# Optimization experiments

Hardware: AMD Instinct MI355X
Metric: run time of the kernel (lower is better)

The kernel has to match this reference:

```python
import jax, jax.numpy as jnp
import numpy as np

N = 100000
E = 640000
ND = 128   # node_dim
ED = 128   # edge_dim
HD = 256   # hidden_dim
EPS = 1e-5


def _mlp_ln(x, W1, b1, W2, b2, W3, b3, g, beta):
    h = jax.nn.relu(x @ W1 + b1)
    h = jax.nn.relu(h @ W2 + b2)
    o = h @ W3 + b3
    mu = jnp.mean(o, axis=-1, keepdims=True)
    var = jnp.mean(jnp.square(o - mu), axis=-1, keepdims=True)
    return (o - mu) * jax.lax.rsqrt(var + EPS) * g + beta


def setup_inputs() -> dict:
    key = jax.random.key(0)
    ks = jax.random.split(key, 20)
    s = 0.02
    inp = {
        "node_emb": jax.random.normal(ks[0], (N, ND), jnp.float32),
        "edge_emb": jax.random.normal(ks[1], (E, ED), jnp.float32),
        "src": jax.random.randint(ks[2], (E,), 0, N),
        "dst": jax.random.randint(ks[3], (E,), 0, N),
        "num_nodes": N,
        # edge MLP: in = 2*ND + ED
        "eW1": jax.random.normal(ks[4], (2 * ND + ED, HD), jnp.float32) * s,
        "eb1": jnp.zeros((HD,), jnp.float32),
        "eW2": jax.random.normal(ks[5], (HD, HD), jnp.float32) * s,
        "eb2": jnp.zeros((HD,), jnp.float32),
        "eW3": jax.random.normal(ks[6], (HD, ED), jnp.float32) * s,
        "eb3": jnp.zeros((ED,), jnp.float32),
        "eg": jnp.ones((ED,), jnp.float32),
        "ebeta": jnp.zeros((ED,), jnp.float32),
        # node MLP: in = ND + ED
        "nW1": jax.random.normal(ks[7], (ND + ED, HD), jnp.float32) * s,
        "nb1": jnp.zeros((HD,), jnp.float32),
        "nW2": jax.random.normal(ks[8], (HD, HD), jnp.float32) * s,
        "nb2": jnp.zeros((HD,), jnp.float32),
        "nW3": jax.random.normal(ks[9], (HD, ND), jnp.float32) * s,
        "nb3": jnp.zeros((ND,), jnp.float32),
        "ng": jnp.ones((ND,), jnp.float32),
        "nbeta": jnp.zeros((ND,), jnp.float32),
    }
    return inp


def reference(node_emb, edge_emb, src, dst, num_nodes,
              eW1, eb1, eW2, eb2, eW3, eb3, eg, ebeta,
              nW1, nb1, nW2, nb2, nW3, nb3, ng, nbeta):
    # Edge update: e' = MLP(concat(h_i, h_j, e)) + e
    edge_input = jnp.concatenate([node_emb[src], node_emb[dst], edge_emb], axis=-1)
    edge_emb_new = _mlp_ln(edge_input, eW1, eb1, eW2, eb2, eW3, eb3, eg, ebeta) + edge_emb
    # Mean aggregation over incoming edges per dst node
    agg = jax.ops.segment_sum(edge_emb_new, dst, num_segments=num_nodes)
    count = jax.ops.segment_sum(jnp.ones((dst.shape[0], 1), node_emb.dtype), dst, num_segments=num_nodes)
    agg = agg / jnp.maximum(count, 1.0)
    # Node update: h' = MLP(concat(h, agg)) + h
    node_input = jnp.concatenate([node_emb, agg], axis=-1)
    node_emb_new = _mlp_ln(node_input, nW1, nb1, nW2, nb2, nW3, nb3, ng, nbeta) + node_emb
    return (node_emb_new, edge_emb_new)
```

## Files before the change

kernel.cpp:

```cpp
#include <hip/hip_runtime.h>
#include <hip/hip_bf16.h>

typedef __attribute__((ext_vector_type(8))) short bf16x8;
typedef __attribute__((ext_vector_type(4))) short s16x4;
typedef __attribute__((ext_vector_type(4))) float f32x4;

__device__ __forceinline__ short f2bf(float f) {
  union { __hip_bfloat16 h; short s; } u;
  u.h = __float2bfloat16(f);
  return u.s;
}

__device__ __forceinline__ void gld_lds16(const short* g, short* l) {
  __builtin_amdgcn_global_load_lds((const __attribute__((address_space(1))) unsigned*)g,
                                   (__attribute__((address_space(3))) unsigned*)l,
                                   16, 0, 0);
}

#define BARX(N) asm volatile("s_waitcnt vmcnt(" #N ") lgkmcnt(0)\ns_barrier" ::: "memory")
#define BARLG() asm volatile("s_waitcnt lgkmcnt(0)\ns_barrier" ::: "memory")

template <bool PERM>
__global__ void prep_kernel(const float* __restrict__ W, short* __restrict__ out, int K, int N) {
  int s = blockIdx.x * 256 + threadIdx.x;
  int NF = N >> 4;
  int total = (K >> 5) * NF * 64;
  if (s >= total) return;
  int l = s & 63, kcf = s >> 6;
  int kc = kcf / NF, f = kcf - kc * NF;
  int kg = l >> 4, l16 = l & 15;
  bf16x8 o;
#pragma unroll
  for (int e = 0; e < 8; ++e) {
    int kh = kc * 32 + kg * 8 + e;
    int k = PERM ? ((kh & ~63) | ((kh & 3) << 4) | ((kh >> 2) & 15)) : kh;
    o[e] = f2bf(W[(size_t)k * N + f * 16 + l16]);
  }
  *(bf16x8*)(out + (size_t)s * 8) = o;
}

__global__ void count_kernel(const int* __restrict__ dst, int* __restrict__ cnt, int E) {
  int i = blockIdx.x * 256 + threadIdx.x;
  if (i < E) atomicAdd(&cnt[dst[i]], 1);
}

__global__ __launch_bounds__(1024) void scan_kernel(const int* __restrict__ cnt,
                                                    int* __restrict__ off,
                                                    int* __restrict__ cursor, int N) {
  __shared__ int wsum[16];
  const int t = threadIdx.x;
  const int w = t >> 6, l = t & 63;
  int running = 0;
  for (int base = 0; base < N; base += 1024) {
    int i = base + t;
    int v = (i < N) ? cnt[i] : 0;
    int x = v;
#pragma unroll
    for (int d = 1; d < 64; d <<= 1) { int y = __shfl_up(x, d); if (l >= d) x += y; }
    if (l == 63) wsum[w] = x;
    __syncthreads();
    if (w == 0) {
      int s = (l < 16) ? wsum[l] : 0;
#pragma unroll
      for (int d = 1; d < 16; d <<= 1) { int y = __shfl_up(s, d); if (l >= d) s += y; }
      if (l < 16) wsum[l] = s;
    }
    __syncthreads();
    int total = wsum[15];
    int wo = (w > 0) ? wsum[w - 1] : 0;
    int excl = running + wo + x - v;
    if (i < N) { off[i] = excl; cursor[i] = excl; }
    running += total;
    __syncthreads();
  }
  if (t == 0) off[N] = running;
}

__global__ void scatter_kernel(const int* __restrict__ dst, int* __restrict__ cursor,
                               int* __restrict__ eidx, int E) {
  int e = blockIdx.x * 256 + threadIdx.x;
  if (e < E) {
    int p = atomicAdd(&cursor[dst[e]], 1);
    eidx[p] = e;
  }
}

__global__ void agg_kernel(const float* __restrict__ edge_out, const int* __restrict__ eidx,
                           const int* __restrict__ off, float* __restrict__ agg, int N) {
  int n = blockIdx.x * 4 + (threadIdx.x >> 6);
  if (n >= N) return;
  int l = threadIdx.x & 63;
  int beg = off[n], end = off[n + 1];
  float ax = 0.f, ay = 0.f;
  int i = beg;
  for (; i + 4 <= end; i += 4) {
    int e0 = eidx[i], e1 = eidx[i + 1], e2 = eidx[i + 2], e3 = eidx[i + 3];
    float2 v0 = *(const float2*)(edge_out + (size_t)e0 * 128 + l * 2);
    float2 v1 = *(const float2*)(edge_out + (size_t)e1 * 128 + l * 2);
    float2 v2 = *(const float2*)(edge_out + (size_t)e2 * 128 + l * 2);
    float2 v3 = *(const float2*)(edge_out + (size_t)e3 * 128 + l * 2);
    ax += v0.x + v1.x + v2.x + v3.x;
    ay += v0.y + v1.y + v2.y + v3.y;
  }
  for (; i < end; ++i) {
    int e = eidx[i];
    float2 v = *(const float2*)(edge_out + (size_t)e * 128 + l * 2);
    ax += v.x; ay += v.y;
  }
  float inv = 1.0f / fmaxf((float)(end - beg), 1.0f);
  *(float2*)(agg + (size_t)n * 128 + l * 2) = make_float2(ax * inv, ay * inv);
}

struct F8 { float4 a, b; };

template <bool IS_EDGE>
__launch_bounds__(512, 2)
__global__ void mlp_kernel(const float* __restrict__ node_emb, const float* __restrict__ edge_emb,
                           const int* __restrict__ src, const int* __restrict__ dst,
                           const short* __restrict__ wAll,
                           const float* __restrict__ b1, const float* __restrict__ b2,
                           const float* __restrict__ b3,
                           const float* __restrict__ gam, const float* __restrict__ bet,
                           const float* __restrict__ agg,
                           float* __restrict__ out_base, int M) {
  extern __shared__ short smem[];
  short* BsBase = smem;
  short* AsBase = smem + 24576;
  short* Hs     = smem + 32768;

  const int tid = threadIdx.x;
  const int m0 = blockIdx.x * 128;
  const int w = tid >> 6, lane = tid & 63, l16 = lane & 15, kg = lane >> 4;
  const int wr = w >> 2, wc = w & 3;

  constexpr int NC1 = IS_EDGE ? 12 : 8;

  const int grow = tid >> 2;
  const int gk = tid & 3;
  const int grc = min(m0 + grow, M - 1);
  const int aslot = (grow >> 4) * 64 + gk * 16 + (grow & 15);
  int gsr = 0, gdr = 0;
  if (IS_EDGE) { gsr = src[grc]; gdr = dst[grc]; }

  float b1v[4], b2v[4];
#pragma unroll
  for (int ct = 0; ct < 4; ++ct) {
    int col = wc * 64 + ct * 16 + l16;
    b1v[ct] = b1[col];
    b2v[ct] = b2[col];
  }
  float b3v[8], gv[8], bev[8];
#pragma unroll
  for (int f = 0; f < 8; ++f) {
    int col = f * 16 + l16;
    b3v[f] = b3[col]; gv[f] = gam[col]; bev[f] = bet[col];
  }

  f32x4 acc[16];
#pragma unroll
  for (int i = 0; i < 16; ++i) { f32x4 z = {0.f, 0.f, 0.f, 0.f}; acc[i] = z; }

  auto bsbuf = [&](int v) -> short* { return BsBase + (size_t)(v % 3) * 8192; };
  auto stage1024 = [&](int v) {
    const short* g = wAll + (size_t)v * 8192;
    short* l = bsbuf(v);
    gld_lds16(g + (size_t)tid * 8, l + (size_t)tid * 8);
    gld_lds16(g + (size_t)(512 + tid) * 8, l + (size_t)(512 + tid) * 8);
  };

  auto gatherA = [&](int c) -> F8 {
    const float* q;
    if (IS_EDGE) {
      if (c < 4)      q = node_emb + (size_t)gsr * 128 + c * 32 + gk * 8;
      else if (c < 8) q = node_emb + (size_t)gdr * 128 + (c - 4) * 32 + gk * 8;
      else            q = edge_emb + (size_t)grc * 128 + (c - 8) * 32 + gk * 8;
    } else {
      if (c < 4) q = node_emb + (size_t)grc * 128 + c * 32 + gk * 8;
      else       q = agg + (size_t)grc * 128 + (c - 4) * 32 + gk * 8;
    }
    F8 r;
    r.a = *(const float4*)q;
    r.b = *(const float4*)(q + 4);
    return r;
  };
  auto writeA = [&](const F8& p, int buf) {
    float t[8];
    *(float4*)t = p.a; *(float4*)(t + 4) = p.b;
    bf16x8 o;
#pragma unroll
    for (int e = 0; e < 8; ++e) o[e] = f2bf(t[e]);
    *(bf16x8*)&AsBase[(size_t)buf * 4096 + (size_t)aslot * 8] = o;
  };

  auto mfma16 = [&](bf16x8* a, bf16x8* b) {
#pragma unroll
    for (int rt = 0; rt < 4; ++rt)
#pragma unroll
      for (int ct = 0; ct < 4; ++ct)
        acc[rt * 4 + ct] = __builtin_amdgcn_mfma_f32_16x16x32_bf16(a[rt], b[ct], acc[rt * 4 + ct], 0, 0, 0);
  };

  auto compA = [&](int i) {
    const short* Ap = AsBase + (size_t)(i & 1) * 4096;
    const short* Bp = bsbuf(i);
    bf16x8 a[4], b[4];
#pragma unroll
    for (int rt = 0; rt < 4; ++rt)
      a[rt] = *(const bf16x8*)&Ap[(size_t)((wr * 4 + rt) * 64 + kg * 16 + l16) * 8];
#pragma unroll
    for (int ct = 0; ct < 4; ++ct)
      b[ct] = *(const bf16x8*)&Bp[(size_t)((wc * 4 + ct) * 64 + lane) * 8];
    mfma16(a, b);
  };

  auto computeH = [&](int j, const short* Bp) {
    bf16x8 a[4], b[4];
#pragma unroll
    for (int rt = 0; rt < 4; ++rt) {
      int row = wr * 64 + rt * 16 + l16;
      int ch = (j * 32 + kg * 8) ^ ((row & 7) << 3);
      a[rt] = *(const bf16x8*)&Hs[(size_t)row * 256 + ch];
    }
#pragma unroll
    for (int ct = 0; ct < 4; ++ct)
      b[ct] = *(const bf16x8*)&Bp[(size_t)((wc * 4 + ct) * 64 + lane) * 8];
    mfma16(a, b);
  };

  auto writeH = [&](const float* bv) {
#pragma unroll
    for (int rt = 0; rt < 4; ++rt)
#pragma unroll
      for (int q = 0; q < 4; ++q) {
        int row = wr * 64 + rt * 16 + kg * 4 + q;
        s16x4 v;
#pragma unroll
        for (int ct = 0; ct < 4; ++ct)
          v[ct] = f2bf(fmaxf(acc[rt * 4 + ct][q] + bv[ct], 0.f));
        int ch = (wc * 64 + l16 * 4) ^ ((row & 7) << 3);
        *(s16x4*)&Hs[(size_t)row * 256 + ch] = v;
      }
#pragma unroll
    for (int i = 0; i < 16; ++i) { f32x4 z = {0.f, 0.f, 0.f, 0.f}; acc[i] = z; }
  };

  auto computeL3 = [&](int kk, const short* Bp) {
    int row = w * 16 + l16;
    int ch = (kk * 32 + kg * 8) ^ ((row & 7) << 3);
    bf16x8 a = *(const bf16x8*)&Hs[(size_t)row * 256 + ch];
    const short* Bsub = Bp + (size_t)(kk & 1) * 4096;
#pragma unroll
    for (int f = 0; f < 8; ++f) {
      bf16x8 b = *(const bf16x8*)&Bsub[(size_t)(f * 64 + lane) * 8];
      acc[f] = __builtin_amdgcn_mfma_f32_16x16x32_bf16(a, b, acc[f], 0, 0, 0);
    }
  };

  F8 hold0 = gatherA(0);
  stage1024(0);
  stage1024(1);
  F8 hold = gatherA(1);
  writeA(hold0, 0);
  BARX(4);

#pragma unroll
  for (int i = 0; i < NC1; ++i) {
    stage1024(i + 2);
    F8 gnew = hold;
    if (i + 2 < NC1) gnew = gatherA(i + 2);
    compA(i);
    if (i + 1 < NC1) writeA(hold, (i + 1) & 1);
    if (i + 2 < NC1) { BARX(4); } else { BARX(2); }
    hold = gnew;
  }
  writeH(b1v);
  BARLG();

#pragma unroll
  for (int j = 0; j < 8; ++j) {
    int p = NC1 + j;
    stage1024(p + 2);
    computeH(j, bsbuf(p));
    BARX(2);
  }
  writeH(b2v);
  BARLG();

#pragma unroll
  for (int k = 0; k < 4; ++k) {
    int p = NC1 + 8 + k;
    if (k < 2) stage1024(p + 2);
    computeL3(2 * k, bsbuf(p));
    computeL3(2 * k + 1, bsbuf(p));
    if (k == 0 || k == 1) { BARX(2); }
    else if (k == 2)      { BARX(0); }
  }

#pragma unroll
  for (int q = 0; q < 4; ++q) {
    int rg = m0 + w * 16 + kg * 4 + q;
    float o[8], s1 = 0.f, s2 = 0.f;
#pragma unroll
    for (int f = 0; f < 8; ++f) {
      float x = acc[f][q] + b3v[f];
      o[f] = x; s1 += x; s2 += x * x;
    }
#pragma unroll
    for (int m = 1; m <= 8; m <<= 1) { s1 += __shfl_xor(s1, m); s2 += __shfl_xor(s2, m); }
    float mu = s1 * (1.f / 128.f);
    float var = s2 * (1.f / 128.f) - mu * mu;
    float rs = rsqrtf(var + 1e-5f);
    if (rg < M) {
      const float* resid = (IS_EDGE ? edge_emb : node_emb) + (size_t)rg * 128;
      float* op = out_base + (size_t)rg * 128;
#pragma unroll
      for (int f = 0; f < 8; ++f) {
        int col = f * 16 + l16;
        op[col] = (o[f] - mu) * rs * gv[f] + bev[f] + resid[col];
      }
    }
  }
}

extern "C" void kernel_launch(void* const* d_in, const int* in_sizes, int n_in,
                              void* d_out, int out_size, void* d_ws, size_t ws_size,
                              hipStream_t stream) {
  const float* node_emb = (const float*)d_in[0];
  const float* edge_emb = (const float*)d_in[1];
  const int*   src      = (const int*)d_in[2];
  const int*   dst      = (const int*)d_in[3];
  const float* eW1 = (const float*)d_in[5];
  const float* eb1 = (const float*)d_in[6];
  const float* eW2 = (const float*)d_in[7];
  const float* eb2 = (const float*)d_in[8];
  const float* eW3 = (const float*)d_in[9];
  const float* eb3 = (const float*)d_in[10];
  const float* eg  = (const float*)d_in[11];
  const float* ebt = (const float*)d_in[12];
  const float* nW1 = (const float*)d_in[13];
  const float* nb1 = (const float*)d_in[14];
  const float* nW2 = (const float*)d_in[15];
  const float* nb2 = (const float*)d_in[16];
  const float* nW3 = (const float*)d_in[17];
  const float* nb3 = (const float*)d_in[18];
  const float* ng  = (const float*)d_in[19];
  const float* nbt = (const float*)d_in[20];

  const int Nn = in_sizes[0] / 128;
  const int Ee = in_sizes[2];

  char* ws = (char*)d_ws;
  float* agg  = (float*)ws;  ws += (size_t)Nn * 128 * 4;
  int* cnt_i  = (int*)ws;    ws += (size_t)Nn * 4;
  int* cursor = (int*)ws;    ws += (size_t)Nn * 4;
  int* offv   = (int*)ws;    ws += (size_t)(Nn + 1) * 4;
  int* eidx   = (int*)ws;    ws += (size_t)Ee * 4;
  ws = (char*)(((uintptr_t)ws + 15) & ~(uintptr_t)15);
  short* wp = (short*)ws;
  short* eAll = wp;
  short* nAll = wp + 196608;

  float* out_node = (float*)d_out;
  float* out_edge = out_node + (size_t)Nn * 128;

  hipMemsetAsync(cnt_i, 0, (size_t)Nn * 4, stream);

  prep_kernel<false><<<48, 256, 0, stream>>>(eW1, eAll, 384, 256);
  prep_kernel<true><<<32, 256, 0, stream>>>(eW2, eAll + 98304, 256, 256);
  prep_kernel<true><<<16, 256, 0, stream>>>(eW3, eAll + 163840, 256, 128);
  prep_kernel<false><<<32, 256, 0, stream>>>(nW1, nAll, 256, 256);
  prep_kernel<true><<<32, 256, 0, stream>>>(nW2, nAll + 65536, 256, 256);
  prep_kernel<true><<<16, 256, 0, stream>>>(nW3, nAll + 131072, 256, 128);

  count_kernel<<<(Ee + 255) / 256, 256, 0, stream>>>(dst, cnt_i, Ee);
  scan_kernel<<<1, 1024, 0, stream>>>(cnt_i, offv, cursor, Nn);
  scatter_kernel<<<(Ee + 255) / 256, 256, 0, stream>>>(dst, cursor, eidx, Ee);

  mlp_kernel<true><<<(Ee + 127) / 128, 512, 131072, stream>>>(
      node_emb, edge_emb, src, dst, eAll,
      eb1, eb2, eb3, eg, ebt, agg, out_edge, Ee);

  agg_kernel<<<(Nn + 3) / 4, 256, 0, stream>>>(out_edge, eidx, offv, agg, Nn);

  mlp_kernel<false><<<(Nn + 127) / 128, 512, 131072, stream>>>(
      node_emb, edge_emb, src, dst, nAll,
      nb1, nb2, nb3, ng, nbt, agg, out_node, Nn);
}
```

Before: 751.8 us.

## Pre-convert node embeddings to bf16, read weights directly from global, split layer-3 across waves

Adds a conversion pass that turns node_emb into bf16, so the edge MLP gathers src/dst rows with direct global-to-LDS loads and half the bytes. The aggregate buffer is also stored in bf16. Weights are no longer staged through a triple-buffered LDS ring; each wave loads its B fragments straight from global/L2 into registers with a two-deep prefetch. Layer 3 is split across all wave columns, with a cross-wave LayerNorm reduction through LDS, and the LDS footprint shrinks. The costs are more global weight traffic per block, an extra barrier for the LayerNorm partial sums, and an extra kernel launch.

Result: slower. 919.2 us (+22.3%).

```diff
diff --git a/kernel.cpp b/kernel.cpp
--- a/kernel.cpp
+++ b/kernel.cpp
@@ -17,8 +17,18 @@
                                    16, 0, 0);
 }
 
-#define BARX(N) asm volatile("s_waitcnt vmcnt(" #N ") lgkmcnt(0)\ns_barrier" ::: "memory")
-#define BARLG() asm volatile("s_waitcnt lgkmcnt(0)\ns_barrier" ::: "memory")
+__global__ void cvt_kernel(const float* __restrict__ in, short* __restrict__ out, long n8) {
+  long i = (long)blockIdx.x * blockDim.x + threadIdx.x;
+  const long stride = (long)gridDim.x * blockDim.x;
+  for (; i < n8; i += stride) {
+    const float* p = in + i * 8;
+    float4 a = *(const float4*)p, b = *(const float4*)(p + 4);
+    bf16x8 o;
+    o[0] = f2bf(a.x); o[1] = f2bf(a.y); o[2] = f2bf(a.z); o[3] = f2bf(a.w);
+    o[4] = f2bf(b.x); o[5] = f2bf(b.y); o[6] = f2bf(b.z); o[7] = f2bf(b.w);
+    *(bf16x8*)(out + i * 8) = o;
+  }
+}
 
 template <bool PERM>
 __global__ void prep_kernel(const float* __restrict__ W, short* __restrict__ out, int K, int N) {
@@ -86,7 +96,7 @@
 }
 
 __global__ void agg_kernel(const float* __restrict__ edge_out, const int* __restrict__ eidx,
-                           const int* __restrict__ off, float* __restrict__ agg, int N) {
+                           const int* __restrict__ off, short* __restrict__ aggb, int N) {
   int n = blockIdx.x * 4 + (threadIdx.x >> 6);
   if (n >= N) return;
   int l = threadIdx.x & 63;
@@ -108,25 +118,25 @@
     ax += v.x; ay += v.y;
   }
   float inv = 1.0f / fmaxf((float)(end - beg), 1.0f);
-  *(float2*)(agg + (size_t)n * 128 + l * 2) = make_float2(ax * inv, ay * inv);
-}
-
-struct F8 { float4 a, b; };
+  unsigned pk = ((unsigned)(unsigned short)f2bf(ay * inv) << 16) |
+                (unsigned)(unsigned short)f2bf(ax * inv);
+  *(unsigned*)&aggb[(size_t)n * 128 + l * 2] = pk;
+}
 
 template <bool IS_EDGE>
 __launch_bounds__(512, 2)
-__global__ void mlp_kernel(const float* __restrict__ node_emb, const float* __restrict__ edge_emb,
+__global__ void mlp_kernel(const float* __restrict__ node_emb_f, const float* __restrict__ edge_emb_f,
+                           const short* __restrict__ node_bf, const short* __restrict__ agg_bf,
                            const int* __restrict__ src, const int* __restrict__ dst,
                            const short* __restrict__ wAll,
                            const float* __restrict__ b1, const float* __restrict__ b2,
                            const float* __restrict__ b3,
                            const float* __restrict__ gam, const float* __restrict__ bet,
-                           const float* __restrict__ agg,
                            float* __restrict__ out_base, int M) {
   extern __shared__ short smem[];
-  short* BsBase = smem;
-  short* AsBase = smem + 24576;
-  short* Hs     = smem + 32768;
+  short* As = smem;
+  short* Hs = smem + 16384;
+  float2* pbuf = (float2*)(smem + 49152);
 
   const int tid = threadIdx.x;
   const int m0 = blockIdx.x * 128;
@@ -134,13 +144,15 @@
   const int wr = w >> 2, wc = w & 3;
 
   constexpr int NC1 = IS_EDGE ? 12 : 8;
-
-  const int grow = tid >> 2;
-  const int gk = tid & 3;
-  const int grc = min(m0 + grow, M - 1);
-  const int aslot = (grow >> 4) * 64 + gk * 16 + (grow & 15);
+  constexpr int NG = NC1 / 2;
+  const short* w2p = wAll + (size_t)NC1 * 8192;
+  const short* w3p = w2p + 8 * 8192;
+
+  const int srow = ((tid >> 6) & 7) * 16 + (tid & 15);
+  const int src_rc = min(m0 + srow, M - 1);
+  const int kgo = ((tid >> 4) & 3) * 8;
   int gsr = 0, gdr = 0;
-  if (IS_EDGE) { gsr = src[grc]; gdr = dst[grc]; }
+  if (IS_EDGE) { gsr = src[src_rc]; gdr = dst[src_rc]; }
 
   float b1v[4], b2v[4];
 #pragma unroll
@@ -149,82 +161,77 @@
     b1v[ct] = b1[col];
     b2v[ct] = b2[col];
   }
-  float b3v[8], gv[8], bev[8];
-#pragma unroll
-  for (int f = 0; f < 8; ++f) {
-    int col = f * 16 + l16;
-    b3v[f] = b3[col]; gv[f] = gam[col]; bev[f] = bet[col];
-  }
 
   f32x4 acc[16];
 #pragma unroll
   for (int i = 0; i < 16; ++i) { f32x4 z = {0.f, 0.f, 0.f, 0.f}; acc[i] = z; }
 
-  auto bsbuf = [&](int v) -> short* { return BsBase + (size_t)(v % 3) * 8192; };
-  auto stage1024 = [&](int v) {
-    const short* g = wAll + (size_t)v * 8192;
-    short* l = bsbuf(v);
-    gld_lds16(g + (size_t)tid * 8, l + (size_t)tid * 8);
-    gld_lds16(g + (size_t)(512 + tid) * 8, l + (size_t)(512 + tid) * 8);
-  };
-
-  auto gatherA = [&](int c) -> F8 {
-    const float* q;
-    if (IS_EDGE) {
-      if (c < 4)      q = node_emb + (size_t)gsr * 128 + c * 32 + gk * 8;
-      else if (c < 8) q = node_emb + (size_t)gdr * 128 + (c - 4) * 32 + gk * 8;
-      else            q = edge_emb + (size_t)grc * 128 + (c - 8) * 32 + gk * 8;
-    } else {
-      if (c < 4) q = node_emb + (size_t)grc * 128 + c * 32 + gk * 8;
-      else       q = agg + (size_t)grc * 128 + (c - 4) * 32 + gk * 8;
-    }
-    F8 r;
-    r.a = *(const float4*)q;
-    r.b = *(const float4*)(q + 4);
-    return r;
-  };
-  auto writeA = [&](const F8& p, int buf) {
-    float t[8];
-    *(float4*)t = p.a; *(float4*)(t + 4) = p.b;
-    bf16x8 o;
-#pragma unroll
-    for (int e = 0; e < 8; ++e) o[e] = f2bf(t[e]);
-    *(bf16x8*)&AsBase[(size_t)buf * 4096 + (size_t)aslot * 8] = o;
-  };
-
-  auto mfma16 = [&](bf16x8* a, bf16x8* b) {
+  auto stageG = [&](int g, int buf) {
+#pragma unroll
+    for (int j = 0; j < 2; ++j) {
+      int cb = g * 64 + j * 32 + kgo;
+      short* ldst = As + (size_t)buf * 8192 + (size_t)(j * 512 + tid) * 8;
+      if (IS_EDGE) {
+        if (cb < 256) {
+          const short* q = node_bf + (size_t)(cb < 128 ? gsr : gdr) * 128 + (cb & 127);
+          gld_lds16(q, ldst);
+        } else {
+          const float* q = edge_emb_f + (size_t)src_rc * 128 + (cb - 256);
+          float4 a = *(const float4*)q, bb = *(const float4*)(q + 4);
+          bf16x8 o;
+          o[0] = f2bf(a.x);  o[1] = f2bf(a.y);  o[2] = f2bf(a.z);  o[3] = f2bf(a.w);
+          o[4] = f2bf(bb.x); o[5] = f2bf(bb.y); o[6] = f2bf(bb.z); o[7] = f2bf(bb.w);
+          *(bf16x8*)ldst = o;
+        }
+      } else {
+        const short* q = (cb < 128) ? node_bf + (size_t)src_rc * 128 + cb
+                                    : agg_bf + (size_t)src_rc * 128 + (cb - 128);
+        gld_lds16(q, ldst);
+      }
+    }
+  };
+
+  auto loadB1 = [&](int kc, bf16x8* bb) {
+#pragma unroll
+    for (int ct = 0; ct < 4; ++ct)
+      bb[ct] = *(const bf16x8*)(wAll + ((size_t)((kc * 16 + wc * 4 + ct) * 64 + lane)) * 8);
+  };
+  auto loadB2 = [&](int kc, bf16x8* bb) {
+#pragma unroll
+    for (int ct = 0; ct < 4; ++ct)
+      bb[ct] = *(const bf16x8*)(w2p + ((size_t)((kc * 16 + wc * 4 + ct) * 64 + lane)) * 8);
+  };
+  auto loadB3 = [&](int kc, bf16x8* bb) {
+#pragma unroll
+    for (int ct = 0; ct < 2; ++ct)
+      bb[ct] = *(const bf16x8*)(w3p + ((size_t)((kc * 8 + wc * 2 + ct) * 64 + lane)) * 8);
+  };
+
+  auto compA = [&](int kcl, int buf, bf16x8* bb) {
+    bf16x8 a[4];
 #pragma unroll
     for (int rt = 0; rt < 4; ++rt)
+      a[rt] = *(const bf16x8*)&As[(size_t)buf * 8192 + (size_t)(kcl * 512 + (wr * 4 + rt) * 64 + lane) * 8];
+#pragma unroll
+    for (int rt = 0; rt < 4; ++rt)
 #pragma unroll
       for (int ct = 0; ct < 4; ++ct)
-        acc[rt * 4 + ct] = __builtin_amdgcn_mfma_f32_16x16x32_bf16(a[rt], b[ct], acc[rt * 4 + ct], 0, 0, 0);
-  };
-
-  auto compA = [&](int i) {
-    const short* Ap = AsBase + (size_t)(i & 1) * 4096;
-    const short* Bp = bsbuf(i);
-    bf16x8 a[4], b[4];
-#pragma unroll
-    for (int rt = 0; rt < 4; ++rt)
-      a[rt] = *(const bf16x8*)&Ap[(size_t)((wr * 4 + rt) * 64 + kg * 16 + l16) * 8];
-#pragma unroll
-    for (int ct = 0; ct < 4; ++ct)
-      b[ct] = *(const bf16x8*)&Bp[(size_t)((wc * 4 + ct) * 64 + lane) * 8];
-    mfma16(a, b);
-  };
-
-  auto computeH = [&](int j, const short* Bp) {
-    bf16x8 a[4], b[4];
+        acc[rt * 4 + ct] = __builtin_amdgcn_mfma_f32_16x16x32_bf16(a[rt], bb[ct], acc[rt * 4 + ct], 0, 0, 0);
+  };
+
+  auto compH = [&](int kc, bf16x8* bb) {
+    bf16x8 a[4];
 #pragma unroll
     for (int rt = 0; rt < 4; ++rt) {
       int row = wr * 64 + rt * 16 + l16;
-      int ch = (j * 32 + kg * 8) ^ ((row & 7) << 3);
+      int ch = (kc * 32 + kg * 8) ^ ((row & 7) << 3);
       a[rt] = *(const bf16x8*)&Hs[(size_t)row * 256 + ch];
     }
 #pragma unroll
-    for (int ct = 0; ct < 4; ++ct)
-      b[ct] = *(const bf16x8*)&Bp[(size_t)((wc * 4 + ct) * 64 + lane) * 8];
-    mfma16(a, b);
+    for (int rt = 0; rt < 4; ++rt)
+#pragma unroll
+      for (int ct = 0; ct < 4; ++ct)
+        acc[rt * 4 + ct] = __builtin_amdgcn_mfma_f32_16x16x32_bf16(a[rt], bb[ct], acc[rt * 4 + ct], 0, 0, 0);
   };
 
   auto writeH = [&](const float* bv) {
@@ -244,82 +251,104 @@
     for (int i = 0; i < 16; ++i) { f32x4 z = {0.f, 0.f, 0.f, 0.f}; acc[i] = z; }
   };
 
-  auto computeL3 = [&](int kk, const short* Bp) {
-    int row = w * 16 + l16;
-    int ch = (kk * 32 + kg * 8) ^ ((row & 7) << 3);
-    bf16x8 a = *(const bf16x8*)&Hs[(size_t)row * 256 + ch];
-    const short* Bsub = Bp + (size_t)(kk & 1) * 4096;
-#pragma unroll
-    for (int f = 0; f < 8; ++f) {
-      bf16x8 b = *(const bf16x8*)&Bsub[(size_t)(f * 64 + lane) * 8];
-      acc[f] = __builtin_amdgcn_mfma_f32_16x16x32_bf16(a, b, acc[f], 0, 0, 0);
-    }
-  };
-
-  F8 hold0 = gatherA(0);
-  stage1024(0);
-  stage1024(1);
-  F8 hold = gatherA(1);
-  writeA(hold0, 0);
-  BARX(4);
-
-#pragma unroll
-  for (int i = 0; i < NC1; ++i) {
-    stage1024(i + 2);
-    F8 gnew = hold;
-    if (i + 2 < NC1) gnew = gatherA(i + 2);
-    compA(i);
-    if (i + 1 < NC1) writeA(hold, (i + 1) & 1);
-    if (i + 2 < NC1) { BARX(4); } else { BARX(2); }
-    hold = gnew;
+  stageG(0, 0);
+  __syncthreads();
+  bf16x8 bc[4], bn[4];
+#pragma unroll
+  for (int g = 0; g < NG; ++g) {
+    if (g + 1 < NG) stageG(g + 1, (g + 1) & 1);
+    loadB1(2 * g, bc);
+    loadB1(2 * g + 1, bn);
+    compA(0, g & 1, bc);
+    compA(1, g & 1, bn);
+    __syncthreads();
   }
   writeH(b1v);
-  BARLG();
-
-#pragma unroll
-  for (int j = 0; j < 8; ++j) {
-    int p = NC1 + j;
-    stage1024(p + 2);
-    computeH(j, bsbuf(p));
-    BARX(2);
-  }
+  __syncthreads();
+
+  loadB2(0, bc);
+  loadB2(1, bn);
+#pragma unroll
+  for (int kc = 0; kc < 8; ++kc) {
+    bf16x8 bnew[4];
+    if (kc + 2 < 8) loadB2(kc + 2, bnew);
+    compH(kc, bc);
+#pragma unroll
+    for (int ct = 0; ct < 4; ++ct) { bc[ct] = bn[ct]; bn[ct] = bnew[ct]; }
+  }
+  __syncthreads();
   writeH(b2v);
-  BARLG();
-
-#pragma unroll
-  for (int k = 0; k < 4; ++k) {
-    int p = NC1 + 8 + k;
-    if (k < 2) stage1024(p + 2);
-    computeL3(2 * k, bsbuf(p));
-    computeL3(2 * k + 1, bsbuf(p));
-    if (k == 0 || k == 1) { BARX(2); }
-    else if (k == 2)      { BARX(0); }
-  }
-
-#pragma unroll
-  for (int q = 0; q < 4; ++q) {
-    int rg = m0 + w * 16 + kg * 4 + q;
-    float o[8], s1 = 0.f, s2 = 0.f;
-#pragma unroll
-    for (int f = 0; f < 8; ++f) {
-      float x = acc[f][q] + b3v[f];
-      o[f] = x; s1 += x; s2 += x * x;
-    }
-#pragma unroll
-    for (int m = 1; m <= 8; m <<= 1) { s1 += __shfl_xor(s1, m); s2 += __shfl_xor(s2, m); }
-    float mu = s1 * (1.f / 128.f);
-    float var = s2 * (1.f / 128.f) - mu * mu;
-    float rs = rsqrtf(var + 1e-5f);
-    if (rg < M) {
-      const float* resid = (IS_EDGE ? edge_emb : node_emb) + (size_t)rg * 128;
-      float* op = out_base + (size_t)rg * 128;
-#pragma unroll
-      for (int f = 0; f < 8; ++f) {
-        int col = f * 16 + l16;
-        op[col] = (o[f] - mu) * rs * gv[f] + bev[f] + resid[col];
+  __syncthreads();
+
+  bf16x8 c0[2], c1[2];
+  loadB3(0, c0);
+  loadB3(1, c1);
+#pragma unroll
+  for (int kc = 0; kc < 8; ++kc) {
+    bf16x8 cn[2];
+    if (kc + 2 < 8) loadB3(kc + 2, cn);
+    bf16x8 a[4];
+#pragma unroll
+    for (int rt = 0; rt < 4; ++rt) {
+      int row = wr * 64 + rt * 16 + l16;
+      int ch = (kc * 32 + kg * 8) ^ ((row & 7) << 3);
+      a[rt] = *(const bf16x8*)&Hs[(size_t)row * 256 + ch];
+    }
+#pragma unroll
+    for (int rt = 0; rt < 4; ++rt)
+#pragma unroll
+      for (int ct = 0; ct < 2; ++ct)
+        acc[rt * 2 + ct] = __builtin_amdgcn_mfma_f32_16x16x32_bf16(a[rt], c0[ct], acc[rt * 2 + ct], 0, 0, 0);
+#pragma unroll
+    for (int ct = 0; ct < 2; ++ct) { c0[ct] = c1[ct]; c1[ct] = cn[ct]; }
+  }
+
+  float b3v[2], gv[2], bev[2];
+#pragma unroll
+  for (int ct = 0; ct < 2; ++ct) {
+    int col = wc * 32 + ct * 16 + l16;
+    b3v[ct] = b3[col]; gv[ct] = gam[col]; bev[ct] = bet[col];
+  }
+#pragma unroll
+  for (int rt = 0; rt < 4; ++rt)
+#pragma unroll
+    for (int q = 0; q < 4; ++q) {
+      int row = wr * 64 + rt * 16 + kg * 4 + q;
+      float x0 = acc[rt * 2 + 0][q] + b3v[0];
+      float x1 = acc[rt * 2 + 1][q] + b3v[1];
+      acc[rt * 2 + 0][q] = x0;
+      acc[rt * 2 + 1][q] = x1;
+      float s1 = x0 + x1, s2 = x0 * x0 + x1 * x1;
+#pragma unroll
+      for (int m = 1; m <= 8; m <<= 1) { s1 += __shfl_xor(s1, m); s2 += __shfl_xor(s2, m); }
+      if (l16 == 0) pbuf[row * 4 + wc] = make_float2(s1, s2);
+    }
+  __syncthreads();
+#pragma unroll
+  for (int rt = 0; rt < 4; ++rt)
+#pragma unroll
+    for (int q = 0; q < 4; ++q) {
+      int row = wr * 64 + rt * 16 + kg * 4 + q;
+      float2 p0 = pbuf[row * 4 + 0];
+      float2 p1 = pbuf[row * 4 + 1];
+      float2 p2 = pbuf[row * 4 + 2];
+      float2 p3 = pbuf[row * 4 + 3];
+      float S1 = p0.x + p1.x + p2.x + p3.x;
+      float S2 = p0.y + p1.y + p2.y + p3.y;
+      float mu = S1 * (1.f / 128.f);
+      float var = S2 * (1.f / 128.f) - mu * mu;
+      float rs = rsqrtf(var + 1e-5f);
+      int rg = m0 + row;
+      if (rg < M) {
+        const float* resid = (IS_EDGE ? edge_emb_f : node_emb_f) + (size_t)rg * 128;
+        float* op = out_base + (size_t)rg * 128;
+#pragma unroll
+        for (int ct = 0; ct < 2; ++ct) {
+          int col = wc * 32 + ct * 16 + l16;
+          op[col] = (acc[rt * 2 + ct][q] - mu) * rs * gv[ct] + bev[ct] + resid[col];
+        }
       }
     }
-  }
 }
 
 extern "C" void kernel_launch(void* const* d_in, const int* in_sizes, int n_in,
@@ -350,20 +379,22 @@
   const int Ee = in_sizes[2];
 
   char* ws = (char*)d_ws;
-  float* agg  = (float*)ws;  ws += (size_t)Nn * 128 * 4;
-  int* cnt_i  = (int*)ws;    ws += (size_t)Nn * 4;
-  int* cursor = (int*)ws;    ws += (size_t)Nn * 4;
-  int* offv   = (int*)ws;    ws += (size_t)(Nn + 1) * 4;
-  int* eidx   = (int*)ws;    ws += (size_t)Ee * 4;
+  short* aggb   = (short*)ws;  ws += (size_t)Nn * 128 * 2;
+  short* nodebf = (short*)ws;  ws += (size_t)Nn * 128 * 2;
+  int* cnt_i  = (int*)ws;      ws += (size_t)Nn * 4;
+  int* cursor = (int*)ws;      ws += (size_t)Nn * 4;
+  int* offv   = (int*)ws;      ws += (size_t)(Nn + 1) * 4;
+  int* eidx   = (int*)ws;      ws += (size_t)Ee * 4;
   ws = (char*)(((uintptr_t)ws + 15) & ~(uintptr_t)15);
-  short* wp = (short*)ws;
-  short* eAll = wp;
-  short* nAll = wp + 196608;
+  short* eAll = (short*)ws;
+  short* nAll = eAll + 196608;
 
   float* out_node = (float*)d_out;
   float* out_edge = out_node + (size_t)Nn * 128;
 
   hipMemsetAsync(cnt_i, 0, (size_t)Nn * 4, stream);
+
+  cvt_kernel<<<2048, 256, 0, stream>>>(node_emb, nodebf, (long)Nn * 16);
 
   prep_kernel<false><<<48, 256, 0, stream>>>(eW1, eAll, 384, 256);
   prep_kernel<true><<<32, 256, 0, stream>>>(eW2, eAll + 98304, 256, 256);
@@ -376,13 +407,13 @@
   scan_kernel<<<1, 1024, 0, stream>>>(cnt_i, offv, cursor, Nn);
   scatter_kernel<<<(Ee + 255) / 256, 256, 0, stream>>>(dst, cursor, eidx, Ee);
 
-  mlp_kernel<true><<<(Ee + 127) / 128, 512, 131072, stream>>>(
-      node_emb, edge_emb, src, dst, eAll,
-      eb1, eb2, eb3, eg, ebt, agg, out_edge, Ee);
-
-  agg_kernel<<<(Nn + 3) / 4, 256, 0, stream>>>(out_edge, eidx, offv, agg, Nn);
-
-  mlp_kernel<false><<<(Nn + 127) / 128, 512, 131072, stream>>>(
-      node_emb, edge_emb, src, dst, nAll,
-      nb1, nb2, nb3, ng, nbt, agg, out_node, Nn);
-}
+  mlp_kernel<true><<<(Ee + 127) / 128, 512, 102400, stream>>>(
+      node_emb, edge_emb, nodebf, aggb, src, dst, eAll,
+      eb1, eb2, eb3, eg, ebt, out_edge, Ee);
+
+  agg_kernel<<<(Nn + 3) / 4, 256, 0, stream>>>(out_edge, eidx, offv, aggb, Nn);
+
+  mlp_kernel<false><<<(Nn + 127) / 128, 512, 102400, stream>>>(
+      node_emb, edge_emb, nodebf, aggb, src, dst, nAll,
+      nb1, nb2, nb3, ng, nbt, out_node, Nn);
+}
```
